# Optimization experiments

Hardware: AMD Instinct MI355X
Metric: run time of the kernel (lower is better)

## Reference

```python
import jax, jax.numpy as jnp
import numpy as np


def setup_inputs() -> dict:
    key = jax.random.key(0)
    ks = jax.random.split(key, 8)
    D = 1024
    B, R, L = 128, 256, 128
    s = 1.0 / np.sqrt(D)
    return {
        "cap_emb": jax.random.normal(ks[0], (L, D), jnp.float32),
        "img_emb": jax.random.normal(ks[1], (B, R, D), jnp.float32),
        "Wq": jax.random.normal(ks[2], (D, D), jnp.float32) * s,
        "bq": jnp.zeros((D,), jnp.float32),
        "Wk": jax.random.normal(ks[3], (D, D), jnp.float32) * s,
        "bk": jnp.zeros((D,), jnp.float32),
        "Wv": jax.random.normal(ks[4], (D, D), jnp.float32) * s,
        "bv": jnp.zeros((D,), jnp.float32),
    }


def reference(cap_emb, img_emb, Wq, bq, Wk, bk, Wv, bv):
    # cap_emb: [L, D] captions, img_emb: [B, R, D] image regions
    D = cap_emb.shape[-1]
    norm_fact = 1.0 / jnp.sqrt(jnp.asarray(D, cap_emb.dtype))
    # Q from captions (shared across batch; avoid the explicit repeat)
    Q = cap_emb @ Wq.T + bq                      # [L, D]
    K = img_emb @ Wk.T + bk                      # [B, R, D]
    V = img_emb @ Wv.T + bv                      # [B, R, D]
    scores = jnp.einsum('ld,brd->blr', Q, K)     # [B, L, R]
    # Faithful to source: scale applied AFTER softmax
    atten = jax.nn.softmax(scores, axis=-1) * norm_fact
    out = jnp.einsum('blr,brd->bld', atten, V)   # [B, L, D]
    return out
```

## Files before the change

kernel.cpp:

```cpp
#include <hip/hip_runtime.h>
#include <stdint.h>

typedef __attribute__((ext_vector_type(4))) float  f32x4;
typedef __attribute__((ext_vector_type(8))) short  s16x8;
typedef __attribute__((ext_vector_type(4))) short  s16x4;
typedef __attribute__((ext_vector_type(4))) unsigned int u32x4;
typedef __attribute__((ext_vector_type(2))) unsigned int u32x2;

__device__ __forceinline__ unsigned short f2bf(float x) {
  union { float f; unsigned int u; } a; a.f = x;
  unsigned int lsb = (a.u >> 16) & 1u;
  a.u += 0x7fffu + lsb;
  return (unsigned short)(a.u >> 16);
}
__device__ __forceinline__ float bf2f(unsigned short h) {
  union { unsigned int u; float f; } a; a.u = ((unsigned int)h) << 16; return a.f;
}
__device__ __forceinline__ unsigned int cvtpk(float a, float b) {
  unsigned int d;
  asm("v_cvt_pk_bf16_f32 %0, %1, %2" : "=v"(d) : "v"(a), "v"(b));
  return d;
}
__device__ __forceinline__ float bflo_f(unsigned int u) {
  union { unsigned int u; float f; } x; x.u = u << 16; return x.f;
}
__device__ __forceinline__ float bfhi_f(unsigned int u) {
  union { unsigned int u; float f; } x; x.u = u & 0xffff0000u; return x.f;
}
__device__ __forceinline__ s16x8 pk4(unsigned a, unsigned b, unsigned c, unsigned d) {
  union { u32x4 u; s16x8 s; } x;
  u32x4 v = {a, b, c, d}; x.u = v; return x.s;
}

__device__ __forceinline__ void gload_lds16(const void* g, void* s) {
  __builtin_amdgcn_global_load_lds(
      (__attribute__((address_space(1))) void*)g,
      (__attribute__((address_space(3))) void*)s, 16, 0, 0);
}

#define VMCNT(N) asm volatile("s_waitcnt vmcnt(" #N ")" ::: "memory")
#define LGKM0()  asm volatile("s_waitcnt lgkmcnt(0)" ::: "memory")
#define SBAR()   __builtin_amdgcn_s_barrier()
#define SFENCE() __builtin_amdgcn_sched_barrier(0)

__global__ __launch_bounds__(256) void k_q_part(
    const float* __restrict__ A, const float* __restrict__ Bm,
    float* __restrict__ Qp) {
  __shared__ float As[32][33], Bs[32][33];
  int tid = threadIdx.x;
  int bm = blockIdx.x * 32, bn = blockIdx.y * 32;
  int kbase = blockIdx.z * 256;
  int tr = tid & 31, tq = tid >> 5;
  float acc[4] = {0.f, 0.f, 0.f, 0.f};
  for (int k0 = kbase; k0 < kbase + 256; k0 += 32) {
#pragma unroll
    for (int i = 0; i < 4; i++) {
      int idx = tid + i * 256;
      int r = idx >> 5, c = idx & 31;
      As[r][c] = A[(size_t)(bm + r) * 1024 + k0 + c];
      Bs[r][c] = Bm[(size_t)(bn + r) * 1024 + k0 + c];
    }
    __syncthreads();
#pragma unroll
    for (int kk = 0; kk < 32; kk++) {
      float b = Bs[tr][kk];
#pragma unroll
      for (int i = 0; i < 4; i++) acc[i] += As[tq * 4 + i][kk] * b;
    }
    __syncthreads();
  }
#pragma unroll
  for (int i = 0; i < 4; i++)
    Qp[(size_t)blockIdx.z * 131072 + (size_t)(bm + tq * 4 + i) * 1024 + bn + tr] = acc[i];
}

__global__ __launch_bounds__(256) void k_qw_part(
    const float* __restrict__ Qp, const float* __restrict__ bq,
    const float* __restrict__ Wk, float* __restrict__ QWp) {
  __shared__ float As[32][33], Bs[32][33];
  int tid = threadIdx.x;
  int bm = blockIdx.x * 32, bn = blockIdx.y * 32;
  int kbase = blockIdx.z * 256;
  int tr = tid & 31, tq = tid >> 5;
  float acc[4] = {0.f, 0.f, 0.f, 0.f};
  for (int k0 = kbase; k0 < kbase + 256; k0 += 32) {
#pragma unroll
    for (int i = 0; i < 4; i++) {
      int idx = tid + i * 256;
      int r = idx >> 5, c = idx & 31;
      size_t qa = (size_t)(bm + r) * 1024 + k0 + c;
      float s = (Qp[qa] + Qp[qa + 131072]) + (Qp[qa + 262144] + Qp[qa + 393216]);
      As[r][c] = s + bq[k0 + c];
      Bs[r][c] = Wk[(size_t)(k0 + r) * 1024 + bn + c];
    }
    __syncthreads();
#pragma unroll
    for (int kk = 0; kk < 32; kk++) {
      float b = Bs[kk][tr];
#pragma unroll
      for (int i = 0; i < 4; i++) acc[i] += As[tq * 4 + i][kk] * b;
    }
    __syncthreads();
  }
#pragma unroll
  for (int i = 0; i < 4; i++)
    QWp[(size_t)blockIdx.z * 131072 + (size_t)(bm + tq * 4 + i) * 1024 + bn + tr] = acc[i];
}

__global__ __launch_bounds__(256) void k_reduce_convert(
    const float* __restrict__ QWp, const float* __restrict__ Wv,
    unsigned short* __restrict__ QWh, unsigned short* __restrict__ QWl,
    unsigned short* __restrict__ Wvh) {
  int bid = blockIdx.x;
  if (bid < 128) {
    int i = bid * 256 + threadIdx.x;
    const f32x4* P4 = (const f32x4*)QWp;
    f32x4 a = P4[i], b = P4[i + 32768], c = P4[i + 65536], d = P4[i + 98304];
    f32x4 s;
#pragma unroll
    for (int j = 0; j < 4; j++) s[j] = (a[j] + b[j]) + (c[j] + d[j]);
    unsigned h0 = cvtpk(s[0], s[1]), h1 = cvtpk(s[2], s[3]);
    unsigned l0 = cvtpk(s[0] - bflo_f(h0), s[1] - bfhi_f(h0));
    unsigned l1 = cvtpk(s[2] - bflo_f(h1), s[3] - bfhi_f(h1));
    u32x2 hv = {h0, h1}, lv = {l0, l1};
    ((u32x2*)QWh)[i] = hv;
    ((u32x2*)QWl)[i] = lv;
  } else {
    int i = (bid - 128) * 256 + threadIdx.x;
    f32x4 v = ((const f32x4*)Wv)[i];
    u32x2 h;
    h[0] = cvtpk(v[0], v[1]);
    h[1] = cvtpk(v[2], v[3]);
    ((u32x2*)Wvh)[i] = h;
  }
}

__global__ __launch_bounds__(512, 2) void k_fused(
    const unsigned short* __restrict__ QWh, const unsigned short* __restrict__ QWl,
    const float* __restrict__ img, unsigned short* __restrict__ Cp) {
  __shared__ __attribute__((aligned(16))) char lds[122880];
  int tid = threadIdx.x, l = tid & 63, w = tid >> 6;
  int wm = w >> 2, wn = w & 3;
  int lr = l & 15, lk8 = l >> 4;
  int sF = (lr >> 1) & 3;
  int rh = lk8 * 4;
  int bid = blockIdx.x;
  int xcd = bid & 7, loc = bid >> 3;
  int b = xcd * 16 + (loc >> 1);
  int lh = loc & 1;
  const int Poff = 81920, RMAX = 114688, RSUM = 115712;

  int arow = (w & 3) * 16 + (l >> 2);
  int achk = (l & 3) ^ ((arow >> 1) & 3);
  const unsigned short* aW = (w < 4) ? QWh : QWl;
  const unsigned short* asrc = aW + (size_t)(lh * 64 + arow) * 1024 + achk * 8;
  int aOff = ((w < 4) ? 0 : 4096) + (w & 3) * 1024;
  int bR0 = tid >> 3;
  int bc  = (tid >> 1) & 3;
  int bb0 = bR0 * 64 + ((bc ^ ((bR0 >> 1) & 3)) << 4) + (tid & 1) * 8;
  const float* gB0 = img + ((size_t)b * 256 + bR0) * 1024 + (tid & 7) * 4;

  char* scur = &lds[0];
  char* snxt = &lds[40960];
  char* snx2 = &lds[81920];
  f32x4 sA0, sA1, sA2, sA3, sB0, sB1, sB2, sB3, sC0, sC1, sC2, sC3;
  f32x4 acc[2][4] = {};

#define SC_LOADB(K0, R0, R1, R2, R3) { \
    R0 = *(const f32x4*)(gB0 + (K0)); \
    R1 = *(const f32x4*)(gB0 + 65536 + (K0)); \
    R2 = *(const f32x4*)(gB0 + 131072 + (K0)); \
    R3 = *(const f32x4*)(gB0 + 196608 + (K0)); }

#define SC_CONV1(DST, V, S) { \
    unsigned h0 = cvtpk((V)[0], (V)[1]), h1 = cvtpk((V)[2], (V)[3]); \
    unsigned q0 = cvtpk((V)[0] - bflo_f(h0), (V)[1] - bfhi_f(h0)); \
    unsigned q1 = cvtpk((V)[2] - bflo_f(h1), (V)[3] - bfhi_f(h1)); \
    u32x2 hv = {h0, h1}, lv = {q0, q1}; \
    *(u32x2*)((DST) + 8192 + bb0 + (S) * 4096) = hv; \
    *(u32x2*)((DST) + 24576 + bb0 + (S) * 4096) = lv; }

#define SC_CONV(DST, V0, V1, V2, V3) { \
    SC_CONV1(DST, V0, 0); \
    SC_CONV1(DST, V1, 1); \
    SC_CONV1(DST, V2, 2); \
    SC_CONV1(DST, V3, 3); }

#define SC_COMPUTE(BUF) { \
    s16x8 ah[2], al2[2], bh[4], bl[4]; \
    _Pragma("unroll") \
    for (int i = 0; i < 2; i++) { \
      int row = wm * 32 + i * 16 + lr; \
      int byte = row * 64 + ((lk8 ^ sF) << 4); \
      ah[i] = *(const s16x8*)((BUF) + byte); \
      al2[i] = *(const s16x8*)((BUF) + 4096 + byte); \
    } \
    _Pragma("unroll") \
    for (int j = 0; j < 4; j++) { \
      int n = wn * 64 + j * 16 + lr; \
      int byte = n * 64 + ((lk8 ^ sF) << 4); \
      bh[j] = *(const s16x8*)((BUF) + 8192 + byte); \
      bl[j] = *(const s16x8*)((BUF) + 24576 + byte); \
    } \
    __builtin_amdgcn_s_setprio(1); \
    _Pragma("unroll") \
    for (int i = 0; i < 2; i++) \
      _Pragma("unroll") \
      for (int j = 0; j < 4; j++) { \
        acc[i][j] = __builtin_amdgcn_mfma_f32_16x16x32_bf16(ah[i], bh[j], acc[i][j], 0, 0, 0); \
        acc[i][j] = __builtin_amdgcn_mfma_f32_16x16x32_bf16(ah[i], bl[j], acc[i][j], 0, 0, 0); \
        acc[i][j] = __builtin_amdgcn_mfma_f32_16x16x32_bf16(al2[i], bh[j], acc[i][j], 0, 0, 0); \
      } \
    __builtin_amdgcn_s_setprio(0); }

#define SC_STEP(T, C0, C1, C2, C3, L0, L1, L2, L3) { \
    int ka = ((T) + 2) * 32; \
    int kb = (((T) + 3 < 32) ? (T) + 3 : 31) * 32; \
    gload_lds16(asrc + ka, snx2 + aOff); \
    SFENCE(); \
    SC_LOADB(kb, L0, L1, L2, L3); \
    SFENCE(); \
    SC_COMPUTE(scur); \
    SC_CONV(snxt, C0, C1, C2, C3); \
    VMCNT(9); \
    LGKM0(); \
    SBAR(); \
    SFENCE(); \
    { char* t_ = scur; scur = snxt; snxt = snx2; snx2 = t_; } }

  gload_lds16(asrc, scur + aOff);
  SFENCE();
  SC_LOADB(0, sA0, sA1, sA2, sA3);
  SFENCE();
  gload_lds16(asrc + 32, snxt + aOff);
  SFENCE();
  SC_LOADB(32, sB0, sB1, sB2, sB3);
  SFENCE();
  SC_LOADB(64, sC0, sC1, sC2, sC3);
  SFENCE();
  SC_CONV(scur, sA0, sA1, sA2, sA3);
  LGKM0();
  SBAR();
  SFENCE();
#pragma unroll 1
  for (int t3 = 0; t3 < 30; t3 += 3) {
    SC_STEP(t3,     sB0, sB1, sB2, sB3, sA0, sA1, sA2, sA3);
    SC_STEP(t3 + 1, sC0, sC1, sC2, sC3, sB0, sB1, sB2, sB3);
    SC_STEP(t3 + 2, sA0, sA1, sA2, sA3, sC0, sC1, sC2, sC3);
  }
  SC_COMPUTE(scur);
  SC_CONV(snxt, sB0, sB1, sB2, sB3);
  VMCNT(0);
  LGKM0();
  SBAR();
  SFENCE();
  { char* t_ = scur; scur = snxt; snxt = snx2; snx2 = t_; }
  SC_COMPUTE(scur);
  SBAR();
  SFENCE();
#undef SC_STEP
#undef SC_COMPUTE
#undef SC_CONV
#undef SC_CONV1
#undef SC_LOADB

  {
#pragma unroll
    for (int i = 0; i < 2; i++)
#pragma unroll
      for (int q = 0; q < 4; q++) {
        float m = fmaxf(fmaxf(acc[i][0][q], acc[i][1][q]),
                        fmaxf(acc[i][2][q], acc[i][3][q]));
#pragma unroll
        for (int s = 1; s < 16; s <<= 1) m = fmaxf(m, __shfl_xor(m, s, 64));
        if (lr == 0)
          *(float*)(lds + RMAX + (wm * 32 + i * 16 + rh + q) * 16 + wn * 4) = m;
      }
    LGKM0();
    SBAR();
#pragma unroll
    for (int i = 0; i < 2; i++)
#pragma unroll
      for (int q = 0; q < 4; q++) {
        int row = wm * 32 + i * 16 + rh + q;
        const float* rm = (const float*)(lds + RMAX + row * 16);
        float g = fmaxf(fmaxf(rm[0], rm[1]), fmaxf(rm[2], rm[3]));
        float ps = 0.f;
#pragma unroll
        for (int j = 0; j < 4; j++) {
          float e = __expf(acc[i][j][q] - g);
          acc[i][j][q] = e;
          ps += e;
        }
#pragma unroll
        for (int s = 1; s < 16; s <<= 1) ps += __shfl_xor(ps, s, 64);
        if (lr == 0) *(float*)(lds + RSUM + row * 16 + wn * 4) = ps;
      }
    LGKM0();
    SBAR();
#pragma unroll
    for (int i = 0; i < 2; i++)
#pragma unroll
      for (int q = 0; q < 4; q++) {
        int row = wm * 32 + i * 16 + rh + q;
        const float* rs = (const float*)(lds + RSUM + row * 16);
        float sc = 0.03125f / (rs[0] + rs[1] + rs[2] + rs[3]);
#pragma unroll
        for (int j = 0; j < 4; j++) {
          int col = wn * 64 + j * 16 + lr;
          int byte = Poff + row * 512 +
                     (((col >> 3) ^ ((row & 7) << 2)) << 4) + (col & 7) * 2;
          *(unsigned short*)(lds + byte) = f2bf(acc[i][j][q] * sc);
        }
      }
    LGKM0();
    SBAR();
    SFENCE();
  }

  {
    int u = tid & 15, dc = tid >> 4;
    const float* gva = img + ((size_t)b * 256 + 2 * u) * 1024 + dc * 8;
    const float* gvb = gva + 1024;
    char* ccur = &lds[0];
    char* cnxt = &lds[16384];
    char* cnx2 = &lds[32768];
    f32x4 cAa, cAb, cAc, cAd, cBa, cBb, cBc, cBd, cCa, cCb, cCc, cCd;
    f32x4 acc2[2][4] = {};

#define CTX_LOAD(T, Ra, Rb, Rc, Rd) { \
    int tt = ((T) < 32) ? (T) : 31; \
    size_t off = (size_t)((tt & 7) * 32) * 1024 + (tt >> 3) * 256; \
    Ra = *(const f32x4*)(gva + off); \
    Rb = *(const f32x4*)(gva + off + 4); \
    Rc = *(const f32x4*)(gvb + off); \
    Rd = *(const f32x4*)(gvb + off + 4); }

#define CTX_CONV(DST, Ra, Rb, Rc, Rd) { \
    _Pragma("unroll") \
    for (int j = 0; j < 8; j++) { \
      float x0 = (j < 4) ? (Ra)[j & 3] : (Rb)[j & 3]; \
      float x1 = (j < 4) ? (Rc)[j & 3] : (Rd)[j & 3]; \
      int dd = dc * 8 + j; \
      unsigned int w32 = cvtpk(x0, x1); \
      int byte = dd * 64 + ((4 * u) ^ (((dd >> 1) & 3) << 4)); \
      *(unsigned int*)((DST) + byte) = w32; \
    } }

#define CTX_MFMA(T) { \
    s16x8 af[2], bf[4]; \
    _Pragma("unroll") \
    for (int i = 0; i < 2; i++) { \
      int row = wm * 32 + i * 16 + lr; \
      int rc = ((T) & 7) * 4 + lk8; \
      int byte = Poff + row * 512 + ((rc ^ ((row & 7) << 2)) << 4); \
      af[i] = *(const s16x8*)(lds + byte); \
    } \
    _Pragma("unroll") \
    for (int j = 0; j < 4; j++) { \
      int n = wn * 64 + j * 16 + lr; \
      int byte = n * 64 + ((lk8 ^ ((n >> 1) & 3)) << 4); \
      bf[j] = *(const s16x8*)(ccur + byte); \
    } \
    __builtin_amdgcn_s_setprio(1); \
    _Pragma("unroll") \
    for (int i = 0; i < 2; i++) \
      _Pragma("unroll") \
      for (int j = 0; j < 4; j++) \
        acc2[i][j] = __builtin_amdgcn_mfma_f32_16x16x32_bf16(af[i], bf[j], acc2[i][j], 0, 0, 0); \
    __builtin_amdgcn_s_setprio(0); }

#define CTX_STORE(T) { \
    int d0c = ((T) >> 3) * 256; \
    _Pragma("unroll") \
    for (int i = 0; i < 2; i++) \
      _Pragma("unroll") \
      for (int q = 0; q < 4; q++) { \
        int gl = lh * 64 + wm * 32 + i * 16 + rh + q; \
        _Pragma("unroll") \
        for (int j = 0; j < 4; j++) { \
          int gn = d0c + wn * 64 + j * 16 + lr; \
          Cp[((size_t)b * 128 + gl) * 1024 + gn] = f2bf(acc2[i][j][q]); \
          acc2[i][j][q] = 0.f; \
        } \
      } }

#define CTX_STEP(T, Ca, Cb, Cc, Cd, La, Lb, Lc, Ld) { \
    CTX_LOAD((T) + 3, La, Lb, Lc, Ld); \
    SFENCE(); \
    CTX_MFMA(T); \
    CTX_CONV(cnxt, Ca, Cb, Cc, Cd); \
    if (((T) & 7) == 7) CTX_STORE(T); \
    LGKM0(); \
    SBAR(); \
    SFENCE(); \
    { char* t_ = ccur; ccur = cnxt; cnxt = cnx2; cnx2 = t_; } }

    CTX_LOAD(0, cAa, cAb, cAc, cAd);
    SFENCE();
    CTX_LOAD(1, cBa, cBb, cBc, cBd);
    SFENCE();
    CTX_LOAD(2, cCa, cCb, cCc, cCd);
    SFENCE();
    CTX_CONV(ccur, cAa, cAb, cAc, cAd);
    LGKM0();
    SBAR();
    SFENCE();
#pragma unroll 1
    for (int t3 = 0; t3 < 30; t3 += 3) {
      CTX_STEP(t3,     cBa, cBb, cBc, cBd, cAa, cAb, cAc, cAd);
      CTX_STEP(t3 + 1, cCa, cCb, cCc, cCd, cBa, cBb, cBc, cBd);
      CTX_STEP(t3 + 2, cAa, cAb, cAc, cAd, cCa, cCb, cCc, cCd);
    }
    CTX_MFMA(30);
    CTX_CONV(cnxt, cBa, cBb, cBc, cBd);
    LGKM0();
    SBAR();
    SFENCE();
    { char* t_ = ccur; ccur = cnxt; cnxt = cnx2; cnx2 = t_; }
    CTX_MFMA(31);
    CTX_STORE(31);
#undef CTX_STEP
#undef CTX_STORE
#undef CTX_MFMA
#undef CTX_CONV
#undef CTX_LOAD
  }
}

__global__ __launch_bounds__(512, 2) void k_gemm_out(
    const unsigned short* __restrict__ A, const unsigned short* __restrict__ Bm,
    const float* __restrict__ bv, float* __restrict__ Out) {
  __shared__ __attribute__((aligned(16))) char lds[73728];
  int tid = threadIdx.x, l = tid & 63, w = tid >> 6;
  int wm = w >> 1, wn = w & 1;
  int rid = blockIdx.x;
  int xcd = rid & 7, lid = rid >> 3;
  int bm = (xcd * 8 + (lid >> 3)) * 256;
  int bn = (lid & 7) * 128;
  int lr = l & 15, lk8 = l >> 4;
  int sF = (lr >> 1) & 3;
  int srow = tid >> 2;
  int swz = (tid & 3) ^ ((tid >> 3) & 3);
  const unsigned short* a0 = A + (size_t)(bm + srow) * 1024 + swz * 8;
  const unsigned short* a1 = A + (size_t)(bm + 128 + srow) * 1024 + swz * 8;
  const unsigned short* b0 = Bm + (size_t)(bn + srow) * 1024 + swz * 8;
  char* cur = &lds[0];
  char* nxt = &lds[24576];
  char* nx2 = &lds[49152];
  f32x4 acc[4][4] = {};

#define OUT_STAGE(KN, BUF) { \
    gload_lds16(a0 + (KN), (BUF) + w * 1024); \
    gload_lds16(a1 + (KN), (BUF) + 8192 + w * 1024); \
    gload_lds16(b0 + (KN), (BUF) + 16384 + w * 1024); }

#define OUT_STEP(T) { \
    int kn = (((T) + 2 < 32) ? (T) + 2 : 31) * 32; \
    OUT_STAGE(kn, nx2); \
    SFENCE(); \
    s16x8 af[4], bf[4]; \
    _Pragma("unroll") \
    for (int i = 0; i < 4; i++) { \
      int byte = (wm * 64 + i * 16 + lr) * 64 + ((lk8 ^ sF) << 4); \
      af[i] = *(const s16x8*)(cur + byte); \
    } \
    _Pragma("unroll") \
    for (int i = 0; i < 4; i++) { \
      int byte = 16384 + (wn * 64 + i * 16 + lr) * 64 + ((lk8 ^ sF) << 4); \
      bf[i] = *(const s16x8*)(cur + byte); \
    } \
    __builtin_amdgcn_s_setprio(1); \
    _Pragma("unroll") \
    for (int i = 0; i < 4; i++) \
      _Pragma("unroll") \
      for (int j = 0; j < 4; j++) \
        acc[i][j] = __builtin_amdgcn_mfma_f32_16x16x32_bf16(af[i], bf[j], acc[i][j], 0, 0, 0); \
    __builtin_amdgcn_s_setprio(0); \
    VMCNT(3); \
    SBAR(); \
    SFENCE(); \
    { char* t_ = cur; cur = nxt; nxt = nx2; nx2 = t_; } }

  OUT_STAGE(0, cur);
  SFENCE();
  OUT_STAGE(32, nxt);
  SFENCE();
  VMCNT(3);
  SBAR();
  SFENCE();

#pragma unroll 1
  for (int t = 0; t < 32; ++t) {
    OUT_STEP(t);
  }

  int rh = (l >> 4) * 4;
#pragma unroll
  for (int i = 0; i < 4; i++)
#pragma unroll
    for (int q = 0; q < 4; q++) {
      int gm = bm + wm * 64 + i * 16 + rh + q;
#pragma unroll
      for (int j = 0; j < 4; j++) {
        int gn = bn + wn * 64 + j * 16 + lr;
        Out[(size_t)gm * 1024 + gn] = acc[i][j][q] + 0.03125f * bv[gn];
      }
    }
#undef OUT_STEP
#undef OUT_STAGE
}

extern "C" void kernel_launch(void* const* d_in, const int* in_sizes, int n_in,
                              void* d_out, int out_size, void* d_ws, size_t ws_size,
                              hipStream_t stream) {
  const float* cap = (const float*)d_in[0];
  const float* img = (const float*)d_in[1];
  const float* Wq  = (const float*)d_in[2];
  const float* bq  = (const float*)d_in[3];
  const float* Wk  = (const float*)d_in[4];
  const float* Wv  = (const float*)d_in[6];
  const float* bv  = (const float*)d_in[7];
  float* out = (float*)d_out;

  char* ws = (char*)d_ws;
  if (ws_size < 40370176ull) return;
  unsigned short* ctx = (unsigned short*)(ws);
  float*          Qp  = (float*)(ws + 33554432);
  float*          QWp = (float*)(ws + 35651584);
  unsigned short* QWh = (unsigned short*)(ws + 37748736);
  unsigned short* QWl = (unsigned short*)(ws + 38010880);
  unsigned short* Wvh = (unsigned short*)(ws + 38273024);

  k_q_part<<<dim3(4, 32, 4), 256, 0, stream>>>(cap, Wq, Qp);
  k_qw_part<<<dim3(4, 32, 4), 256, 0, stream>>>(Qp, bq, Wk, QWp);
  k_reduce_convert<<<1152, 256, 0, stream>>>(QWp, Wv, QWh, QWl, Wvh);
  k_fused<<<256, 512, 0, stream>>>(QWh, QWl, img, ctx);
  k_gemm_out<<<512, 512, 0, stream>>>(ctx, Wvh, bv, out);
}
```

Baseline: 154.6 us.

## Process two context tiles per barrier phase with four-slot LDS ring

```diff
diff --git a/kernel.cpp b/kernel.cpp
--- a/kernel.cpp
+++ b/kernel.cpp
@@ -322,10 +322,8 @@
     int u = tid & 15, dc = tid >> 4;
     const float* gva = img + ((size_t)b * 256 + 2 * u) * 1024 + dc * 8;
     const float* gvb = gva + 1024;
-    char* ccur = &lds[0];
-    char* cnxt = &lds[16384];
-    char* cnx2 = &lds[32768];
-    f32x4 cAa, cAb, cAc, cAd, cBa, cBb, cBc, cBd, cCa, cCb, cCc, cCd;
+    f32x4 cA0, cA1, cA2, cA3, cA4, cA5, cA6, cA7;
+    f32x4 cB0, cB1, cB2, cB3, cB4, cB5, cB6, cB7;
     f32x4 acc2[2][4] = {};
 
 #define CTX_LOAD(T, Ra, Rb, Rc, Rd) { \
@@ -336,7 +334,8 @@
     Rc = *(const f32x4*)(gvb + off); \
     Rd = *(const f32x4*)(gvb + off + 4); }
 
-#define CTX_CONV(DST, Ra, Rb, Rc, Rd) { \
+#define CTX_CONV(T, Ra, Rb, Rc, Rd) { \
+    char* dst = lds + ((T) & 3) * 16384; \
     _Pragma("unroll") \
     for (int j = 0; j < 8; j++) { \
       float x0 = (j < 4) ? (Ra)[j & 3] : (Rb)[j & 3]; \
@@ -344,10 +343,11 @@
       int dd = dc * 8 + j; \
       unsigned int w32 = cvtpk(x0, x1); \
       int byte = dd * 64 + ((4 * u) ^ (((dd >> 1) & 3) << 4)); \
-      *(unsigned int*)((DST) + byte) = w32; \
+      *(unsigned int*)(dst + byte) = w32; \
     } }
 
 #define CTX_MFMA(T) { \
+    const char* src = lds + ((T) & 3) * 16384; \
     s16x8 af[2], bf[4]; \
     _Pragma("unroll") \
     for (int i = 0; i < 2; i++) { \
@@ -360,7 +360,7 @@
     for (int j = 0; j < 4; j++) { \
       int n = wn * 64 + j * 16 + lr; \
       int byte = n * 64 + ((lk8 ^ ((n >> 1) & 3)) << 4); \
-      bf[j] = *(const s16x8*)(ccur + byte); \
+      bf[j] = *(const s16x8*)(src + byte); \
     } \
     __builtin_amdgcn_s_setprio(1); \
     _Pragma("unroll") \
@@ -385,42 +385,38 @@
         } \
       } }
 
-#define CTX_STEP(T, Ca, Cb, Cc, Cd, La, Lb, Lc, Ld) { \
-    CTX_LOAD((T) + 3, La, Lb, Lc, Ld); \
+#define CTX_PHASE(P, L0,L1,L2,L3,L4,L5,L6,L7, C0,C1,C2,C3,C4,C5,C6,C7) { \
+    CTX_LOAD(2*(P)+4, L0, L1, L2, L3); \
+    CTX_LOAD(2*(P)+5, L4, L5, L6, L7); \
     SFENCE(); \
-    CTX_MFMA(T); \
-    CTX_CONV(cnxt, Ca, Cb, Cc, Cd); \
-    if (((T) & 7) == 7) CTX_STORE(T); \
+    CTX_MFMA(2*(P)); \
+    CTX_MFMA(2*(P)+1); \
+    CTX_CONV(2*(P)+2, C0, C1, C2, C3); \
+    CTX_CONV(2*(P)+3, C4, C5, C6, C7); \
+    if (((2*(P)+1) & 7) == 7) CTX_STORE(2*(P)+1); \
     LGKM0(); \
     SBAR(); \
-    SFENCE(); \
-    { char* t_ = ccur; ccur = cnxt; cnxt = cnx2; cnx2 = t_; } }
-
-    CTX_LOAD(0, cAa, cAb, cAc, cAd);
+    SFENCE(); }
+
+    CTX_LOAD(0, cA0, cA1, cA2, cA3);
+    CTX_LOAD(1, cA4, cA5, cA6, cA7);
     SFENCE();
-    CTX_LOAD(1, cBa, cBb, cBc, cBd);
+    CTX_LOAD(2, cB0, cB1, cB2, cB3);
+    CTX_LOAD(3, cB4, cB5, cB6, cB7);
     SFENCE();
-    CTX_LOAD(2, cCa, cCb, cCc, cCd);
-    SFENCE();
-    CTX_CONV(ccur, cAa, cAb, cAc, cAd);
+    CTX_CONV(0, cA0, cA1, cA2, cA3);
+    CTX_CONV(1, cA4, cA5, cA6, cA7);
     LGKM0();
     SBAR();
     SFENCE();
 #pragma unroll 1
-    for (int t3 = 0; t3 < 30; t3 += 3) {
-      CTX_STEP(t3,     cBa, cBb, cBc, cBd, cAa, cAb, cAc, cAd);
-      CTX_STEP(t3 + 1, cCa, cCb, cCc, cCd, cBa, cBb, cBc, cBd);
-      CTX_STEP(t3 + 2, cAa, cAb, cAc, cAd, cCa, cCb, cCc, cCd);
+    for (int pp = 0; pp < 16; pp += 2) {
+      CTX_PHASE(pp,     cA0,cA1,cA2,cA3,cA4,cA5,cA6,cA7,
+                        cB0,cB1,cB2,cB3,cB4,cB5,cB6,cB7);
+      CTX_PHASE(pp + 1, cB0,cB1,cB2,cB3,cB4,cB5,cB6,cB7,
+                        cA0,cA1,cA2,cA3,cA4,cA5,cA6,cA7);
     }
-    CTX_MFMA(30);
-    CTX_CONV(cnxt, cBa, cBb, cBc, cBd);
-    LGKM0();
-    SBAR();
-    SFENCE();
-    { char* t_ = ccur; ccur = cnxt; cnxt = cnx2; cnx2 = t_; }
-    CTX_MFMA(31);
-    CTX_STORE(31);
-#undef CTX_STEP
+#undef CTX_PHASE
 #undef CTX_STORE
 #undef CTX_MFMA
 #undef CTX_CONV
```

Measured after the change: 157.6 us. No clear change (+2.0%).
